# Optimization experiments

Measured on AMD Instinct MI355X. Metric: run time of the kernel, lower is better.

Reference implementation:

```python
import jax, jax.numpy as jnp
import numpy as np

N = 4096
IN_F = 128
OUT_F = 64      # per-head out_features
HEADS = 4
ALPHA = 0.2     # LeakyReLU negative slope
NEG_FILL = -9e15


def setup_inputs() -> dict:
    key = jax.random.key(0)
    k_h, k_adj, k_W, k_a = jax.random.split(key, 4)
    h = jax.random.normal(k_h, (N, IN_F), dtype=jnp.float32)
    adj = jax.random.randint(k_adj, (N, N), 0, 2, dtype=jnp.int32)
    W = jax.random.normal(k_W, (IN_F, OUT_F * HEADS), dtype=jnp.float32) * 0.1
    a = jax.random.normal(k_a, (2 * OUT_F, 1), dtype=jnp.float32) * 0.1
    bias = jnp.zeros((OUT_F * HEADS,), dtype=jnp.float32)
    return {"h": h, "adj": adj, "W": W, "a": a, "bias": bias}


def reference(h, adj, W, a, bias):
    n = h.shape[0]
    Wh = (h @ W).reshape(n, HEADS, OUT_F)            # (N, H, F)
    # e_ij = leakyrelu(a_left . Wh_i + a_right . Wh_j)  (decomposed outer sum;
    # same math as concat([Wh_i, Wh_j]) @ a in the original)
    a_left = a[:OUT_F, 0]                            # (F,)
    a_right = a[OUT_F:, 0]                           # (F,)
    left = jnp.einsum('nhf,f->nh', Wh, a_left)       # (N, H)
    right = jnp.einsum('nhf,f->nh', Wh, a_right)     # (N, H)
    mask = adj > 0                                   # (N, N)
    outs = []
    for head in range(HEADS):                        # small fixed loop over heads
        e = left[:, head, None] + right[None, :, head]          # (N, N)
        e = jnp.where(e >= 0, e, ALPHA * e)                      # LeakyReLU
        e = jnp.where(mask, e, NEG_FILL)
        attn = jax.nn.softmax(e, axis=1)                         # (N, N)
        outs.append(attn @ Wh[:, head, :])                       # (N, F)
    out = jnp.concatenate(outs, axis=1)              # concat=True -> (N, H*F)
    return out + bias
```

## Files before the change

kernel.cpp:

```cpp
#include <hip/hip_runtime.h>
#include <hip/hip_bf16.h>

#define NN 4096
#define IN_F 128
#define OUT_F 64
#define C_TOT 256
#define ALPHA 0.2f
#define LOG2E 1.4426950408889634f

typedef float f32x4 __attribute__((ext_vector_type(4)));
typedef float f32x2 __attribute__((ext_vector_type(2)));
typedef __bf16 bf16x8 __attribute__((ext_vector_type(8)));

__device__ __forceinline__ unsigned fmap(float f) {
    unsigned u = __float_as_uint(f);
    return (u >> 31) ? ~u : (u | 0x80000000u);
}
__device__ __forceinline__ float funmap(unsigned u) {
    return (u >> 31) ? __uint_as_float(u & 0x7FFFFFFFu) : __uint_as_float(~u);
}
__device__ __forceinline__ unsigned short bfbits(float x) {
    union { __bf16 b; unsigned short u; } t;
    t.b = (__bf16)x;
    return t.u;
}
__device__ __forceinline__ void gl16(const void* g, void* l) {
    __builtin_amdgcn_global_load_lds((const __attribute__((address_space(1))) void*)g,
                                     (__attribute__((address_space(3))) void*)l, 16, 0, 0);
}

__global__ __launch_bounds__(256) void k_mask(
    const int* __restrict__ adj, unsigned* __restrict__ mask,
    const float* __restrict__ W, const float* __restrict__ a,
    unsigned short* __restrict__ WTbf, float* __restrict__ uLR,
    unsigned int* __restrict__ Rmax)
{
    const int tid = threadIdx.x;
    const int lane = tid & 63, wv = tid >> 6;
    const int row = blockIdx.x * 4 + wv;
    const int* __restrict__ ar = adj + (size_t)row * NN;
    unsigned* __restrict__ mr = mask + (size_t)row * 128;
    for (int c = 0; c < 8; ++c) {
        const int j0 = c * 512;
        unsigned w = 0u;
#pragma unroll
        for (int k = 0; k < 8; ++k) {
            const unsigned long long bb = __ballot(ar[j0 + k * 64 + lane] > 0);
            const unsigned lo = (unsigned)bb, hi = (unsigned)(bb >> 32);
            if ((lane >> 1) == k) w = (lane & 1) ? hi : lo;
        }
        if (lane < 16) {
            const int wi = c * 16 + lane;
            mr[(wi & 3) * 32 + (wi >> 2)] = w;
        }
    }

    if (blockIdx.x < 32) {
        const int b = blockIdx.x;
        const int c = b * 8 + (tid & 7);
#pragma unroll
        for (int pass = 0; pass < 4; ++pass) {
            const int k = pass * 32 + (tid >> 3);
            WTbf[(size_t)c * IN_F + k] = bfbits(W[k * C_TOT + c]);
        }
        if (b == 0) {
            if (tid < 4) Rmax[tid] = 0u;
            for (int o = tid; o < 1024; o += 256) {
                const int k = o >> 3, j = o & 7;
                const int hd = j & 3, side = j >> 2;
                float s = 0.f;
                for (int f = 0; f < OUT_F; ++f)
                    s = fmaf(W[k * C_TOT + hd * OUT_F + f], a[side * OUT_F + f], s);
                uLR[k * 8 + side * 4 + hd] = s;
            }
        }
    }
}

__global__ __launch_bounds__(256) void k_prep(
    const float* __restrict__ hmat, const unsigned short* __restrict__ WTbf,
    const float* __restrict__ uLR, unsigned short* __restrict__ WhT,
    float* __restrict__ leftT, float* __restrict__ rightT,
    unsigned int* __restrict__ Rmax)
{
    __shared__ float hs[16][132];
    __shared__ float us[128][8];
    const int tid = threadIdx.x;
    const int rowbase = blockIdx.x * 16;

    ((float4*)us)[tid] = ((const float4*)uLR)[tid];
#pragma unroll
    for (int p = 0; p < 8; ++p) {
        const int idx = p * 256 + tid;
        hs[idx >> 7][idx & 127] = hmat[(size_t)rowbase * IN_F + idx];
    }
    __syncthreads();

    const int lane = tid & 63, wv = tid >> 6;
    const int m16 = lane & 15, kg = lane >> 4;

    if (wv == 0) {
        const int row = lane >> 2, hd = lane & 3;
        float aL = 0.f, aR = 0.f;
#pragma unroll
        for (int k = 0; k < 128; k += 4) {
            const float4 hv = *(const float4*)&hs[row][k];
            aL = fmaf(hv.x, us[k][hd],   fmaf(hv.y, us[k+1][hd],   fmaf(hv.z, us[k+2][hd],   fmaf(hv.w, us[k+3][hd],   aL))));
            aR = fmaf(hv.x, us[k][hd+4], fmaf(hv.y, us[k+1][hd+4], fmaf(hv.z, us[k+2][hd+4], fmaf(hv.w, us[k+3][hd+4], aR))));
        }
        leftT [hd * NN + rowbase + row] = aL;
        rightT[hd * NN + rowbase + row] = aR * LOG2E;
        float mx = aR;
#pragma unroll
        for (int s = 4; s < 64; s <<= 1) mx = fmaxf(mx, __shfl_xor(mx, s, 64));
        if (lane < 4) atomicMax(&Rmax[hd], fmap(mx));
    }

    bf16x8 afr[4];
#pragma unroll
    for (int ks = 0; ks < 4; ++ks) {
        const float4 lo = *(const float4*)&hs[m16][ks * 32 + kg * 8];
        const float4 hi = *(const float4*)&hs[m16][ks * 32 + kg * 8 + 4];
        bf16x8 v;
        v[0] = (__bf16)lo.x; v[1] = (__bf16)lo.y; v[2] = (__bf16)lo.z; v[3] = (__bf16)lo.w;
        v[4] = (__bf16)hi.x; v[5] = (__bf16)hi.y; v[6] = (__bf16)hi.z; v[7] = (__bf16)hi.w;
        afr[ks] = v;
    }

#pragma unroll
    for (int nt0 = 0; nt0 < 4; ++nt0) {
        const int col = (wv * 4 + nt0) * 16 + m16;
        f32x4 acc = (f32x4){0.f, 0.f, 0.f, 0.f};
#pragma unroll
        for (int ks = 0; ks < 4; ++ks) {
            union { uint4 u; bf16x8 v; } B;
            B.u = *(const uint4*)(WTbf + (size_t)col * IN_F + ks * 32 + kg * 8);
            acc = __builtin_amdgcn_mfma_f32_16x16x32_bf16(afr[ks], B.v, acc, 0, 0, 0);
        }
#pragma unroll
        for (int i = 0; i < 4; ++i)
            WhT[(size_t)col * NN + rowbase + kg * 4 + i] = bfbits(acc[i]);
    }
}

__global__ __launch_bounds__(512, 6) void k_attn(
    const unsigned* __restrict__ mask,
    const unsigned short* __restrict__ WhT,
    const float* __restrict__ leftT,
    const float* __restrict__ rightT,
    const unsigned int* __restrict__ Rmax,
    const float* __restrict__ bias,
    float* __restrict__ out)
{
    __shared__ unsigned short Bb[2][64 * 128];
    __shared__ float rlds[4096];

    const int tid = threadIdx.x;
    const int lane = tid & 63;
    const int wv = tid >> 6;
    const int rh = wv & 1;
    const int j4 = wv >> 1;
    const int rowbase = (blockIdx.x >> 2) * 32;
    const int hd = blockIdx.x & 3;
    const int m = lane & 15;
    const int kg = lane >> 4;
    const int sh = kg * 8;

#pragma unroll
    for (int p = 0; p < 2; ++p) {
        const int i = p * 512 + tid;
        *(float4*)&rlds[i * 4] = *(const float4*)(rightT + (size_t)hd * NN + i * 4);
    }
    unsigned mreg[32];
    {
        const unsigned* mrow = mask + (size_t)(rowbase + rh * 16 + m) * 128 + j4 * 32;
#pragma unroll
        for (int p = 0; p < 8; ++p) {
            const uint4 v = *(const uint4*)(mrow + p * 4);
            mreg[p * 4 + 0] = v.x; mreg[p * 4 + 1] = v.y;
            mreg[p * 4 + 2] = v.z; mreg[p * 4 + 3] = v.w;
        }
    }

    const float lf = leftT[hd * NN + rowbase + rh * 16 + m];
    const float rmx = funmap(Rmax[hd]);
    const float x = lf + rmx;
    const float m0v = fmaxf(x, ALPHA * x);
    const float mp0 = m0v * LOG2E;
    const float lf2 = fmaf(lf, LOG2E, -mp0);
    const float qc = -0.8f * mp0;
    const f32x2 lf22 = (f32x2){lf2, lf2};
    const f32x2 al2  = (f32x2){ALPHA, ALPHA};
    const f32x2 qc2  = (f32x2){qc, qc};

    bf16x8 ONE8;
#pragma unroll
    for (int i = 0; i < 8; ++i) ONE8[i] = (__bf16)1.0f;

    const int srow0 = wv * 4 + (lane >> 4);
    const int g_lin = lane & 15;
    const int lg = g_lin ^ (srow0 & 15);
    const unsigned short* gsrc0 = WhT + (size_t)(hd * 64 + srow0) * NN + lg * 8;
    const unsigned short* gsrc1 = gsrc0 + (size_t)32 * NN;
    const int d0 = wv * 512 + lane * 8;

#define STAGE(buf, t) {                                  \
    gl16(gsrc0 + (t) * 128, &Bb[buf][d0]);               \
    gl16(gsrc1 + (t) * 128, &Bb[buf][4096 + d0]); }

    const int pg8 = ((j4 * 4 + kg) ^ m) * 8;
    const int bro = m * 128 + pg8;

    f32x4 acc0 = (f32x4){0,0,0,0}, acc1 = acc0, acc2 = acc0, acc3 = acc0;
    f32x4 accL = (f32x4){0,0,0,0};

    union F4 { f32x4 v; f32x2 h[2]; };

#define COMPUTE(buf, t) {                                                        \
    const unsigned aw = mreg[(t)] >> sh;                                         \
    F4 RA, RB;                                                                   \
    RA.v = *(const f32x4*)&rlds[(t) * 128 + j4 * 32 + sh];                       \
    RB.v = *(const f32x4*)&rlds[(t) * 128 + j4 * 32 + sh + 4];                   \
    const f32x2 rp2[4] = { RA.h[0], RA.h[1], RB.h[0], RB.h[1] };                 \
    union { __bf16 b[8]; bf16x8 v; } Af;                                         \
    _Pragma("unroll")                                                            \
    for (int e = 0; e < 4; ++e) {                                                \
        const f32x2 p = rp2[e] + lf22;                         \
        const f32x2 q = __builtin_elementwise_fma(p, al2, qc2);    \
        const float t0 = fmaxf(p.x, q.x), t1 = fmaxf(p.y, q.y);                  \
        float w0 = exp2f(t0), w1 = exp2f(t1);                                    \
        const unsigned mk0 = (unsigned)(((int)(aw << (31 - 2*e)))     >> 31);    \
        const unsigned mk1 = (unsigned)(((int)(aw << (31 - (2*e+1)))) >> 31);    \
        w0 = __uint_as_float(__float_as_uint(w0) & mk0);                         \
        w1 = __uint_as_float(__float_as_uint(w1) & mk1);                         \
        Af.b[2*e]   = (__bf16)w0;                                                \
        Af.b[2*e+1] = (__bf16)w1;                                                \
    }                                                                            \
    union { uint4 u; bf16x8 v; } B0, B1, B2, B3;                                 \
    B0.u = *(const uint4*)&Bb[buf][bro];                                         \
    B1.u = *(const uint4*)&Bb[buf][bro + 2048];                                  \
    B2.u = *(const uint4*)&Bb[buf][bro + 4096];                                  \
    B3.u = *(const uint4*)&Bb[buf][bro + 6144];                                  \
    acc0 = __builtin_amdgcn_mfma_f32_16x16x32_bf16(Af.v, B0.v, acc0, 0, 0, 0);   \
    acc1 = __builtin_amdgcn_mfma_f32_16x16x32_bf16(Af.v, B1.v, acc1, 0, 0, 0);   \
    acc2 = __builtin_amdgcn_mfma_f32_16x16x32_bf16(Af.v, B2.v, acc2, 0, 0, 0);   \
    acc3 = __builtin_amdgcn_mfma_f32_16x16x32_bf16(Af.v, B3.v, acc3, 0, 0, 0);   \
    accL = __builtin_amdgcn_mfma_f32_16x16x32_bf16(Af.v, ONE8, accL, 0, 0, 0);   \
}

    STAGE(0, 0);
    __syncthreads();

#pragma unroll
    for (int t = 0; t < 32; ++t) {
        if (t + 1 < 32) {
            STAGE((t + 1) & 1, t + 1);
            asm volatile("s_waitcnt vmcnt(2)" ::: "memory");
        } else {
            asm volatile("s_waitcnt vmcnt(0)" ::: "memory");
        }
        __builtin_amdgcn_sched_barrier(0);
        COMPUTE(t & 1, t);
        __builtin_amdgcn_sched_barrier(0);
        __builtin_amdgcn_s_barrier();
    }
#undef STAGE
#undef COMPUTE

    __syncthreads();
    float* comb = (float*)&Bb[0][0];
    if (j4 > 0) {
        float* c = comb + (((j4 - 1) * 2 + rh) * 64 + lane) * 20;
#pragma unroll
        for (int i = 0; i < 4; ++i) {
            c[ 0 + i] = acc0[i]; c[ 4 + i] = acc1[i];
            c[ 8 + i] = acc2[i]; c[12 + i] = acc3[i];
            c[16 + i] = accL[i];
        }
    }
    __syncthreads();
    if (j4 == 0) {
#pragma unroll
        for (int pt = 0; pt < 3; ++pt) {
            const float* c = comb + ((pt * 2 + rh) * 64 + lane) * 20;
#pragma unroll
            for (int i = 0; i < 4; ++i) {
                acc0[i] += c[ 0 + i]; acc1[i] += c[ 4 + i];
                acc2[i] += c[ 8 + i]; acc3[i] += c[12 + i];
                accL[i] += c[16 + i];
            }
        }
#pragma unroll
        for (int q = 0; q < 4; ++q) {
            const f32x4 A = (q == 0) ? acc0 : (q == 1) ? acc1 : (q == 2) ? acc2 : acc3;
            const int col = hd * 64 + q * 16 + m;
            const float bv = bias[col];
#pragma unroll
            for (int i = 0; i < 4; ++i) {
                const int r = kg * 4 + i;
                out[(size_t)(rowbase + rh * 16 + r) * C_TOT + col] = A[i] / accL[i] + bv;
            }
        }
    }
}

extern "C" void kernel_launch(void* const* d_in, const int* in_sizes, int n_in,
                              void* d_out, int out_size, void* d_ws, size_t ws_size,
                              hipStream_t stream) {
    const float* hmat = (const float*)d_in[0];
    const int*   adj  = (const int*)d_in[1];
    const float* W    = (const float*)d_in[2];
    const float* a    = (const float*)d_in[3];
    const float* bias = (const float*)d_in[4];
    float* out = (float*)d_out;

    char* ws = (char*)d_ws;
    unsigned short* WhT  = (unsigned short*)(ws + 0x000000);
    float* rightT        = (float*)(ws + 0x280000);
    float* leftT         = (float*)(ws + 0x2A0000);
    unsigned short* WTbf = (unsigned short*)(ws + 0x2B0000);
    float* uLR           = (float*)(ws + 0x2C0000);
    unsigned int* Rmax   = (unsigned int*)(ws + 0x2C1000);
    unsigned* mask       = (unsigned*)(ws + 0x300000);

    hipLaunchKernelGGL(k_mask, dim3(1024), dim3(256), 0, stream,
                       adj, mask, W, a, WTbf, uLR, Rmax);
    hipLaunchKernelGGL(k_prep, dim3(256),  dim3(256), 0, stream,
                       hmat, WTbf, uLR, WhT, leftT, rightT, Rmax);
    hipLaunchKernelGGL(k_attn, dim3(512),  dim3(512), 0, stream,
                       mask, WhT, leftT, rightT, Rmax, bias, out);
}
```

Measured before the change: 71.41 us.

## Split attention key range across two blocks with separate finalize kernel

Splits the column (j) dimension of the attention kernel into two halves, doubling the grid to 1024 blocks. Each block writes unnormalized numerators and row denominators to workspace, and a new finalize kernel sums the halves, divides and adds bias. The aim is more parallelism and occupancy on the 256-CU device, helped by halved LDS for the right vector and a raised launch-bounds occupancy hint. The cost is an extra kernel launch plus extra global traffic for the partial results.

```diff
diff --git a/kernel.cpp b/kernel.cpp
--- a/kernel.cpp
+++ b/kernel.cpp
@@ -143,39 +143,39 @@
     }
 }
 
-__global__ __launch_bounds__(512, 6) void k_attn(
+__global__ __launch_bounds__(512, 8) void k_attn(
     const unsigned* __restrict__ mask,
     const unsigned short* __restrict__ WhT,
     const float* __restrict__ leftT,
     const float* __restrict__ rightT,
     const unsigned int* __restrict__ Rmax,
-    const float* __restrict__ bias,
-    float* __restrict__ out)
+    float* __restrict__ out,
+    float* __restrict__ num1,
+    float* __restrict__ den)
 {
     __shared__ unsigned short Bb[2][64 * 128];
-    __shared__ float rlds[4096];
+    __shared__ float rlds[2048];
 
     const int tid = threadIdx.x;
     const int lane = tid & 63;
     const int wv = tid >> 6;
     const int rh = wv & 1;
     const int j4 = wv >> 1;
-    const int rowbase = (blockIdx.x >> 2) * 32;
-    const int hd = blockIdx.x & 3;
+    const int jh = blockIdx.x & 1;
+    const int hd = (blockIdx.x >> 1) & 3;
+    const int rowbase = (blockIdx.x >> 3) * 32;
     const int m = lane & 15;
     const int kg = lane >> 4;
     const int sh = kg * 8;
 
-#pragma unroll
-    for (int p = 0; p < 2; ++p) {
-        const int i = p * 512 + tid;
-        *(float4*)&rlds[i * 4] = *(const float4*)(rightT + (size_t)hd * NN + i * 4);
-    }
-    unsigned mreg[32];
+    *(float4*)&rlds[tid * 4] =
+        *(const float4*)(rightT + (size_t)hd * NN + jh * 2048 + tid * 4);
+    unsigned mreg[16];
     {
-        const unsigned* mrow = mask + (size_t)(rowbase + rh * 16 + m) * 128 + j4 * 32;
-#pragma unroll
-        for (int p = 0; p < 8; ++p) {
+        const unsigned* mrow = mask + (size_t)(rowbase + rh * 16 + m) * 128
+                               + j4 * 32 + jh * 16;
+#pragma unroll
+        for (int p = 0; p < 4; ++p) {
             const uint4 v = *(const uint4*)(mrow + p * 4);
             mreg[p * 4 + 0] = v.x; mreg[p * 4 + 1] = v.y;
             mreg[p * 4 + 2] = v.z; mreg[p * 4 + 3] = v.w;
@@ -200,7 +200,8 @@
     const int srow0 = wv * 4 + (lane >> 4);
     const int g_lin = lane & 15;
     const int lg = g_lin ^ (srow0 & 15);
-    const unsigned short* gsrc0 = WhT + (size_t)(hd * 64 + srow0) * NN + lg * 8;
+    const unsigned short* gsrc0 = WhT + (size_t)(hd * 64 + srow0) * NN
+                                  + jh * 2048 + lg * 8;
     const unsigned short* gsrc1 = gsrc0 + (size_t)32 * NN;
     const int d0 = wv * 512 + lane * 8;
 
@@ -225,8 +226,8 @@
     union { __bf16 b[8]; bf16x8 v; } Af;                                         \
     _Pragma("unroll")                                                            \
     for (int e = 0; e < 4; ++e) {                                                \
-        const f32x2 p = rp2[e] + lf22;                         \
-        const f32x2 q = __builtin_elementwise_fma(p, al2, qc2);    \
+        const f32x2 p = rp2[e] + lf22;                                           \
+        const f32x2 q = __builtin_elementwise_fma(p, al2, qc2);                  \
         const float t0 = fmaxf(p.x, q.x), t1 = fmaxf(p.y, q.y);                  \
         float w0 = exp2f(t0), w1 = exp2f(t1);                                    \
         const unsigned mk0 = (unsigned)(((int)(aw << (31 - 2*e)))     >> 31);    \
@@ -252,8 +253,8 @@
     __syncthreads();
 
 #pragma unroll
-    for (int t = 0; t < 32; ++t) {
-        if (t + 1 < 32) {
+    for (int t = 0; t < 16; ++t) {
+        if (t + 1 < 16) {
             STAGE((t + 1) & 1, t + 1);
             asm volatile("s_waitcnt vmcnt(2)" ::: "memory");
         } else {
@@ -290,18 +291,43 @@
                 accL[i] += c[16 + i];
             }
         }
+        float* numdst = jh ? num1 : out;
 #pragma unroll
         for (int q = 0; q < 4; ++q) {
             const f32x4 A = (q == 0) ? acc0 : (q == 1) ? acc1 : (q == 2) ? acc2 : acc3;
             const int col = hd * 64 + q * 16 + m;
-            const float bv = bias[col];
 #pragma unroll
             for (int i = 0; i < 4; ++i) {
                 const int r = kg * 4 + i;
-                out[(size_t)(rowbase + rh * 16 + r) * C_TOT + col] = A[i] / accL[i] + bv;
+                numdst[(size_t)(rowbase + rh * 16 + r) * C_TOT + col] = A[i];
             }
         }
-    }
+        if (m == 0) {
+#pragma unroll
+            for (int i = 0; i < 4; ++i)
+                den[(size_t)jh * 4 * NN + hd * NN + rowbase + rh * 16 + kg * 4 + i] = accL[i];
+        }
+    }
+}
+
+__global__ __launch_bounds__(256) void k_fin(
+    float* __restrict__ out, const float* __restrict__ num1,
+    const float* __restrict__ den, const float* __restrict__ bias)
+{
+    const int idx = blockIdx.x * 256 + threadIdx.x;
+    const int row = idx >> 6;
+    const int c4 = (idx & 63) * 4;
+    const int hd = c4 >> 6;
+    const float d = den[hd * NN + row] + den[4 * NN + hd * NN + row];
+    const float rd = 1.0f / d;
+    float4 n0 = *(float4*)(out + (size_t)row * C_TOT + c4);
+    const float4 n1 = *(const float4*)(num1 + (size_t)row * C_TOT + c4);
+    const float4 bv = *(const float4*)(bias + c4);
+    n0.x = fmaf(n0.x + n1.x, rd, bv.x);
+    n0.y = fmaf(n0.y + n1.y, rd, bv.y);
+    n0.z = fmaf(n0.z + n1.z, rd, bv.z);
+    n0.w = fmaf(n0.w + n1.w, rd, bv.w);
+    *(float4*)(out + (size_t)row * C_TOT + c4) = n0;
 }
 
 extern "C" void kernel_launch(void* const* d_in, const int* in_sizes, int n_in,
@@ -322,11 +348,15 @@
     float* uLR           = (float*)(ws + 0x2C0000);
     unsigned int* Rmax   = (unsigned int*)(ws + 0x2C1000);
     unsigned* mask       = (unsigned*)(ws + 0x300000);
+    float* num1          = (float*)(ws + 0x500000);
+    float* den           = (float*)(ws + 0x900000);
 
     hipLaunchKernelGGL(k_mask, dim3(1024), dim3(256), 0, stream,
                        adj, mask, W, a, WTbf, uLR, Rmax);
     hipLaunchKernelGGL(k_prep, dim3(256),  dim3(256), 0, stream,
                        hmat, WTbf, uLR, WhT, leftT, rightT, Rmax);
-    hipLaunchKernelGGL(k_attn, dim3(512),  dim3(512), 0, stream,
-                       mask, WhT, leftT, rightT, Rmax, bias, out);
-}
+    hipLaunchKernelGGL(k_attn, dim3(1024), dim3(512), 0, stream,
+                       mask, WhT, leftT, rightT, Rmax, out, num1, den);
+    hipLaunchKernelGGL(k_fin,  dim3(1024), dim3(256), 0, stream,
+                       out, num1, den, bias);
+}
```

After: 71.34 us. No clear change (-0.1%).

## Factor exp into precomputed per-node terms, split-K attention with final reduction kernel

Applied to the files above, without the earlier changes.

Replaces the per-element exp2 of the LeakyReLU score with products of precomputed exponentials: exp(l+r) and exp(alpha(l+r)) are split into per-row and per-column factors, and their max is taken since exp is monotonic. The attention kernel is restructured so each block handles 64 rows across four 16-row groups over a quarter of the columns. Mask words and exp factors are streamed through LDS with async loads, using a new mask layout. Partial numerators and denominators go to workspace and a new k_fin kernel sums them and normalizes. This removes the transcendental bottleneck and raises MFMA reuse of B tiles, at the cost of extra global traffic for partial sums, an extra launch, and a risk of overflow or underflow in the factored exponentials.

```diff
diff --git a/kernel.cpp b/kernel.cpp
--- a/kernel.cpp
+++ b/kernel.cpp
@@ -9,7 +9,6 @@
 #define LOG2E 1.4426950408889634f
 
 typedef float f32x4 __attribute__((ext_vector_type(4)));
-typedef float f32x2 __attribute__((ext_vector_type(2)));
 typedef __bf16 bf16x8 __attribute__((ext_vector_type(8)));
 
 __device__ __forceinline__ unsigned fmap(float f) {
@@ -28,9 +27,13 @@
     __builtin_amdgcn_global_load_lds((const __attribute__((address_space(1))) void*)g,
                                      (__attribute__((address_space(3))) void*)l, 16, 0, 0);
 }
+__device__ __forceinline__ void gl4(const void* g, void* l) {
+    __builtin_amdgcn_global_load_lds((const __attribute__((address_space(1))) void*)g,
+                                     (__attribute__((address_space(3))) void*)l, 4, 0, 0);
+}
 
 __global__ __launch_bounds__(256) void k_mask(
-    const int* __restrict__ adj, unsigned* __restrict__ mask,
+    const int* __restrict__ adj, unsigned* __restrict__ mask2,
     const float* __restrict__ W, const float* __restrict__ a,
     unsigned short* __restrict__ WTbf, float* __restrict__ uLR,
     unsigned int* __restrict__ Rmax)
@@ -39,7 +42,7 @@
     const int lane = tid & 63, wv = tid >> 6;
     const int row = blockIdx.x * 4 + wv;
     const int* __restrict__ ar = adj + (size_t)row * NN;
-    unsigned* __restrict__ mr = mask + (size_t)row * 128;
+    const int rg = row >> 6, r64 = row & 63;
     for (int c = 0; c < 8; ++c) {
         const int j0 = c * 512;
         unsigned w = 0u;
@@ -51,7 +54,8 @@
         }
         if (lane < 16) {
             const int wi = c * 16 + lane;
-            mr[(wi & 3) * 32 + (wi >> 2)] = w;
+            const int jq = wi >> 5, t = (wi >> 2) & 7, j4 = wi & 3;
+            mask2[(size_t)(((rg * 4 + jq) * 8) + t) * 256 + r64 * 4 + j4] = w;
         }
     }
 
@@ -80,7 +84,7 @@
 __global__ __launch_bounds__(256) void k_prep(
     const float* __restrict__ hmat, const unsigned short* __restrict__ WTbf,
     const float* __restrict__ uLR, unsigned short* __restrict__ WhT,
-    float* __restrict__ leftT, float* __restrict__ rightT,
+    float* __restrict__ leftT, float2* __restrict__ erPair,
     unsigned int* __restrict__ Rmax)
 {
     __shared__ float hs[16][132];
@@ -108,8 +112,9 @@
             aL = fmaf(hv.x, us[k][hd],   fmaf(hv.y, us[k+1][hd],   fmaf(hv.z, us[k+2][hd],   fmaf(hv.w, us[k+3][hd],   aL))));
             aR = fmaf(hv.x, us[k][hd+4], fmaf(hv.y, us[k+1][hd+4], fmaf(hv.z, us[k+2][hd+4], fmaf(hv.w, us[k+3][hd+4], aR))));
         }
-        leftT [hd * NN + rowbase + row] = aL;
-        rightT[hd * NN + rowbase + row] = aR * LOG2E;
+        leftT[hd * NN + rowbase + row] = aL;
+        const float rp = aR * LOG2E;
+        erPair[(size_t)hd * NN + rowbase + row] = make_float2(exp2f(rp), exp2f(ALPHA * rp));
         float mx = aR;
 #pragma unroll
         for (int s = 4; s < 64; s <<= 1) mx = fmaxf(mx, __shfl_xor(mx, s, 64));
@@ -143,119 +148,119 @@
     }
 }
 
-__global__ __launch_bounds__(512, 6) void k_attn(
-    const unsigned* __restrict__ mask,
+__global__ __launch_bounds__(256, 3) void k_attn(
+    const unsigned* __restrict__ mask2,
     const unsigned short* __restrict__ WhT,
     const float* __restrict__ leftT,
-    const float* __restrict__ rightT,
+    const float2* __restrict__ erPair,
     const unsigned int* __restrict__ Rmax,
-    const float* __restrict__ bias,
-    float* __restrict__ out)
+    float* __restrict__ out,
+    float* __restrict__ num123,
+    float* __restrict__ den)
 {
     __shared__ unsigned short Bb[2][64 * 128];
-    __shared__ float rlds[4096];
+    __shared__ float erb[2][256];
+    __shared__ unsigned mb[2][256];
 
     const int tid = threadIdx.x;
     const int lane = tid & 63;
-    const int wv = tid >> 6;
-    const int rh = wv & 1;
-    const int j4 = wv >> 1;
-    const int rowbase = (blockIdx.x >> 2) * 32;
-    const int hd = blockIdx.x & 3;
+    const int j4 = tid >> 6;
+    const int jq = blockIdx.x & 3;
+    const int hd = (blockIdx.x >> 2) & 3;
+    const int rg = blockIdx.x >> 4;
+    const int rowbase = rg * 64;
     const int m = lane & 15;
     const int kg = lane >> 4;
     const int sh = kg * 8;
 
-#pragma unroll
-    for (int p = 0; p < 2; ++p) {
-        const int i = p * 512 + tid;
-        *(float4*)&rlds[i * 4] = *(const float4*)(rightT + (size_t)hd * NN + i * 4);
-    }
-    unsigned mreg[32];
-    {
-        const unsigned* mrow = mask + (size_t)(rowbase + rh * 16 + m) * 128 + j4 * 32;
-#pragma unroll
-        for (int p = 0; p < 8; ++p) {
-            const uint4 v = *(const uint4*)(mrow + p * 4);
-            mreg[p * 4 + 0] = v.x; mreg[p * 4 + 1] = v.y;
-            mreg[p * 4 + 2] = v.z; mreg[p * 4 + 3] = v.w;
-        }
-    }
-
-    const float lf = leftT[hd * NN + rowbase + rh * 16 + m];
+    const int srow4 = j4 * 4 + (lane >> 4);
+    const int g_lin = lane & 15;
+    const int lg = g_lin ^ srow4;
+    const unsigned short* gB = WhT + (size_t)(hd * 64 + srow4) * NN + jq * 1024 + lg * 8;
+    const int dB = srow4 * 128 + g_lin * 8;
+    const char* gE = (const char*)(erPair + (size_t)hd * NN + jq * 1024);
+    const char* gM = (const char*)mask2 + (size_t)((rg * 4 + jq) * 8) * 1024;
+    char* eDst = (char*)&erb[0][0];
+    char* mDst = (char*)&mb[0][0];
+
+#define STAGE(buf, t) {                                                        \
+    gl16(gB + (t) * 128,                      &Bb[buf][dB]);                   \
+    gl16(gB + (t) * 128 + (size_t)16 * NN,    &Bb[buf][dB + 2048]);            \
+    gl16(gB + (t) * 128 + (size_t)32 * NN,    &Bb[buf][dB + 4096]);            \
+    gl16(gB + (t) * 128 + (size_t)48 * NN,    &Bb[buf][dB + 6144]);            \
+    gl4(gE + (t) * 1024 + tid * 4, eDst + (buf) * 1024 + j4 * 256 + lane * 4); \
+    gl4(gM + (t) * 1024 + tid * 4, mDst + (buf) * 1024 + j4 * 256 + lane * 4); }
+
+    STAGE(0, 0);
+
     const float rmx = funmap(Rmax[hd]);
-    const float x = lf + rmx;
-    const float m0v = fmaxf(x, ALPHA * x);
-    const float mp0 = m0v * LOG2E;
-    const float lf2 = fmaf(lf, LOG2E, -mp0);
-    const float qc = -0.8f * mp0;
-    const f32x2 lf22 = (f32x2){lf2, lf2};
-    const f32x2 al2  = (f32x2){ALPHA, ALPHA};
-    const f32x2 qc2  = (f32x2){qc, qc};
-
+    float EL[4], EL2[4];
+#pragma unroll
+    for (int rh = 0; rh < 4; ++rh) {
+        const float lf = leftT[hd * NN + rowbase + rh * 16 + m];
+        const float x = lf + rmx;
+        const float mp0 = fmaxf(x, ALPHA * x) * LOG2E;
+        EL [rh] = exp2f(fmaf(lf,         LOG2E, -mp0));
+        EL2[rh] = exp2f(fmaf(lf * ALPHA, LOG2E, -mp0));
+    }
     bf16x8 ONE8;
 #pragma unroll
     for (int i = 0; i < 8; ++i) ONE8[i] = (__bf16)1.0f;
-
-    const int srow0 = wv * 4 + (lane >> 4);
-    const int g_lin = lane & 15;
-    const int lg = g_lin ^ (srow0 & 15);
-    const unsigned short* gsrc0 = WhT + (size_t)(hd * 64 + srow0) * NN + lg * 8;
-    const unsigned short* gsrc1 = gsrc0 + (size_t)32 * NN;
-    const int d0 = wv * 512 + lane * 8;
-
-#define STAGE(buf, t) {                                  \
-    gl16(gsrc0 + (t) * 128, &Bb[buf][d0]);               \
-    gl16(gsrc1 + (t) * 128, &Bb[buf][4096 + d0]); }
 
     const int pg8 = ((j4 * 4 + kg) ^ m) * 8;
     const int bro = m * 128 + pg8;
 
-    f32x4 acc0 = (f32x4){0,0,0,0}, acc1 = acc0, acc2 = acc0, acc3 = acc0;
-    f32x4 accL = (f32x4){0,0,0,0};
-
-    union F4 { f32x4 v; f32x2 h[2]; };
-
-#define COMPUTE(buf, t) {                                                        \
-    const unsigned aw = mreg[(t)] >> sh;                                         \
-    F4 RA, RB;                                                                   \
-    RA.v = *(const f32x4*)&rlds[(t) * 128 + j4 * 32 + sh];                       \
-    RB.v = *(const f32x4*)&rlds[(t) * 128 + j4 * 32 + sh + 4];                   \
-    const f32x2 rp2[4] = { RA.h[0], RA.h[1], RB.h[0], RB.h[1] };                 \
-    union { __bf16 b[8]; bf16x8 v; } Af;                                         \
-    _Pragma("unroll")                                                            \
-    for (int e = 0; e < 4; ++e) {                                                \
-        const f32x2 p = rp2[e] + lf22;                         \
-        const f32x2 q = __builtin_elementwise_fma(p, al2, qc2);    \
-        const float t0 = fmaxf(p.x, q.x), t1 = fmaxf(p.y, q.y);                  \
-        float w0 = exp2f(t0), w1 = exp2f(t1);                                    \
-        const unsigned mk0 = (unsigned)(((int)(aw << (31 - 2*e)))     >> 31);    \
-        const unsigned mk1 = (unsigned)(((int)(aw << (31 - (2*e+1)))) >> 31);    \
-        w0 = __uint_as_float(__float_as_uint(w0) & mk0);                         \
-        w1 = __uint_as_float(__float_as_uint(w1) & mk1);                         \
-        Af.b[2*e]   = (__bf16)w0;                                                \
-        Af.b[2*e+1] = (__bf16)w1;                                                \
-    }                                                                            \
-    union { uint4 u; bf16x8 v; } B0, B1, B2, B3;                                 \
-    B0.u = *(const uint4*)&Bb[buf][bro];                                         \
-    B1.u = *(const uint4*)&Bb[buf][bro + 2048];                                  \
-    B2.u = *(const uint4*)&Bb[buf][bro + 4096];                                  \
-    B3.u = *(const uint4*)&Bb[buf][bro + 6144];                                  \
-    acc0 = __builtin_amdgcn_mfma_f32_16x16x32_bf16(Af.v, B0.v, acc0, 0, 0, 0);   \
-    acc1 = __builtin_amdgcn_mfma_f32_16x16x32_bf16(Af.v, B1.v, acc1, 0, 0, 0);   \
-    acc2 = __builtin_amdgcn_mfma_f32_16x16x32_bf16(Af.v, B2.v, acc2, 0, 0, 0);   \
-    acc3 = __builtin_amdgcn_mfma_f32_16x16x32_bf16(Af.v, B3.v, acc3, 0, 0, 0);   \
-    accL = __builtin_amdgcn_mfma_f32_16x16x32_bf16(Af.v, ONE8, accL, 0, 0, 0);   \
-}
-
-    STAGE(0, 0);
+    f32x4 acc[4][4], accL[4];
+#pragma unroll
+    for (int rh = 0; rh < 4; ++rh) {
+        accL[rh] = (f32x4){0,0,0,0};
+#pragma unroll
+        for (int q = 0; q < 4; ++q) acc[rh][q] = (f32x4){0,0,0,0};
+    }
+
     __syncthreads();
 
-#pragma unroll
-    for (int t = 0; t < 32; ++t) {
-        if (t + 1 < 32) {
+#define COMPUTE(buf, t) {                                                      \
+    unsigned aw[4];                                                            \
+    _Pragma("unroll")                                                          \
+    for (int rh = 0; rh < 4; ++rh)                                             \
+        aw[rh] = mb[buf][(rh * 16 + m) * 4 + j4] >> sh;                        \
+    const char* eb = (const char*)&erb[buf][0] + j4 * 256 + kg * 64;           \
+    f32x4 V[4];                                                                \
+    _Pragma("unroll")                                                          \
+    for (int c = 0; c < 4; ++c) V[c] = *(const f32x4*)(eb + c * 16);           \
+    union { __bf16 b[8]; bf16x8 v; } Af[4];                                    \
+    _Pragma("unroll")                                                          \
+    for (int rh = 0; rh < 4; ++rh) {                                           \
+        _Pragma("unroll")                                                      \
+        for (int c = 0; c < 4; ++c) {                                          \
+            float w0 = fmaxf(V[c].x * EL[rh], V[c].y * EL2[rh]);               \
+            float w1 = fmaxf(V[c].z * EL[rh], V[c].w * EL2[rh]);               \
+            const unsigned mk0 = (unsigned)(((int)(aw[rh] << (31 - 2*c)))     >> 31); \
+            const unsigned mk1 = (unsigned)(((int)(aw[rh] << (31 - (2*c+1)))) >> 31); \
+            w0 = __uint_as_float(__float_as_uint(w0) & mk0);                   \
+            w1 = __uint_as_float(__float_as_uint(w1) & mk1);                   \
+            Af[rh].b[2*c]   = (__bf16)w0;                                      \
+            Af[rh].b[2*c+1] = (__bf16)w1;                                      \
+        }                                                                      \
+    }                                                                          \
+    union { uint4 u; bf16x8 v; } B[4];                                         \
+    _Pragma("unroll")                                                          \
+    for (int q = 0; q < 4; ++q) B[q].u = *(const uint4*)&Bb[buf][bro + q*2048];\
+    _Pragma("unroll")                                                          \
+    for (int rh = 0; rh < 4; ++rh) {                                           \
+        _Pragma("unroll")                                                      \
+        for (int q = 0; q < 4; ++q)                                            \
+            acc[rh][q] = __builtin_amdgcn_mfma_f32_16x16x32_bf16(Af[rh].v, B[q].v, acc[rh][q], 0, 0, 0); \
+        accL[rh] = __builtin_amdgcn_mfma_f32_16x16x32_bf16(Af[rh].v, ONE8, accL[rh], 0, 0, 0); \
+    }                                                                          \
+}
+
+#pragma unroll
+    for (int t = 0; t < 8; ++t) {
+        if (t < 7) {
             STAGE((t + 1) & 1, t + 1);
-            asm volatile("s_waitcnt vmcnt(2)" ::: "memory");
+            asm volatile("s_waitcnt vmcnt(6)" ::: "memory");
         } else {
             asm volatile("s_waitcnt vmcnt(0)" ::: "memory");
         }
@@ -269,39 +274,74 @@
 
     __syncthreads();
     float* comb = (float*)&Bb[0][0];
-    if (j4 > 0) {
-        float* c = comb + (((j4 - 1) * 2 + rh) * 64 + lane) * 20;
-#pragma unroll
-        for (int i = 0; i < 4; ++i) {
-            c[ 0 + i] = acc0[i]; c[ 4 + i] = acc1[i];
-            c[ 8 + i] = acc2[i]; c[12 + i] = acc3[i];
-            c[16 + i] = accL[i];
-        }
-    }
-    __syncthreads();
+#pragma unroll
+    for (int p = 1; p < 4; ++p) {
+        if (j4 == p) {
+#pragma unroll
+            for (int rh = 0; rh < 4; ++rh) {
+#pragma unroll
+                for (int q = 0; q < 4; ++q)
+                    *(f32x4*)&comb[((rh * 4 + q) * 64 + lane) * 4] = acc[rh][q];
+                *(f32x4*)&comb[((16 + rh) * 64 + lane) * 4] = accL[rh];
+            }
+        }
+        __syncthreads();
+        if (j4 == 0) {
+#pragma unroll
+            for (int rh = 0; rh < 4; ++rh) {
+#pragma unroll
+                for (int q = 0; q < 4; ++q)
+                    acc[rh][q] += *(const f32x4*)&comb[((rh * 4 + q) * 64 + lane) * 4];
+                accL[rh] += *(const f32x4*)&comb[((16 + rh) * 64 + lane) * 4];
+            }
+        }
+        __syncthreads();
+    }
+
     if (j4 == 0) {
-#pragma unroll
-        for (int pt = 0; pt < 3; ++pt) {
-            const float* c = comb + ((pt * 2 + rh) * 64 + lane) * 20;
-#pragma unroll
-            for (int i = 0; i < 4; ++i) {
-                acc0[i] += c[ 0 + i]; acc1[i] += c[ 4 + i];
-                acc2[i] += c[ 8 + i]; acc3[i] += c[12 + i];
-                accL[i] += c[16 + i];
+        float* numdst = (jq == 0) ? out : (num123 + (size_t)(jq - 1) * NN * C_TOT);
+#pragma unroll
+        for (int rh = 0; rh < 4; ++rh) {
+#pragma unroll
+            for (int q = 0; q < 4; ++q) {
+                const int col = hd * 64 + q * 16 + m;
+#pragma unroll
+                for (int i = 0; i < 4; ++i)
+                    numdst[(size_t)(rowbase + rh * 16 + kg * 4 + i) * C_TOT + col] = acc[rh][q][i];
             }
         }
-#pragma unroll
-        for (int q = 0; q < 4; ++q) {
-            const f32x4 A = (q == 0) ? acc0 : (q == 1) ? acc1 : (q == 2) ? acc2 : acc3;
-            const int col = hd * 64 + q * 16 + m;
-            const float bv = bias[col];
-#pragma unroll
-            for (int i = 0; i < 4; ++i) {
-                const int r = kg * 4 + i;
-                out[(size_t)(rowbase + rh * 16 + r) * C_TOT + col] = A[i] / accL[i] + bv;
-            }
-        }
-    }
+        if (m == 0) {
+#pragma unroll
+            for (int rh = 0; rh < 4; ++rh)
+#pragma unroll
+                for (int i = 0; i < 4; ++i)
+                    den[(size_t)(jq * 4 + hd) * NN + rowbase + rh * 16 + kg * 4 + i] = accL[rh][i];
+        }
+    }
+}
+
+__global__ __launch_bounds__(256) void k_fin(
+    float* __restrict__ out, const float* __restrict__ num123,
+    const float* __restrict__ den, const float* __restrict__ bias)
+{
+    const int idx = blockIdx.x * 256 + threadIdx.x;
+    const int row = idx >> 6;
+    const int c4 = (idx & 63) * 4;
+    const int hd = c4 >> 6;
+    const float d = den[(0 * 4 + hd) * NN + row] + den[(1 * 4 + hd) * NN + row]
+                  + den[(2 * 4 + hd) * NN + row] + den[(3 * 4 + hd) * NN + row];
+    const float rd = 1.0f / d;
+    const size_t off = (size_t)row * C_TOT + c4;
+    float4 n = *(float4*)(out + off);
+    const float4 n1 = *(const float4*)(num123 + off);
+    const float4 n2 = *(const float4*)(num123 + (size_t)NN * C_TOT + off);
+    const float4 n3 = *(const float4*)(num123 + (size_t)2 * NN * C_TOT + off);
+    const float4 bv = *(const float4*)(bias + c4);
+    n.x = fmaf(n.x + n1.x + n2.x + n3.x, rd, bv.x);
+    n.y = fmaf(n.y + n1.y + n2.y + n3.y, rd, bv.y);
+    n.z = fmaf(n.z + n1.z + n2.z + n3.z, rd, bv.z);
+    n.w = fmaf(n.w + n1.w + n2.w + n3.w, rd, bv.w);
+    *(float4*)(out + off) = n;
 }
 
 extern "C" void kernel_launch(void* const* d_in, const int* in_sizes, int n_in,
@@ -316,17 +356,21 @@
 
     char* ws = (char*)d_ws;
     unsigned short* WhT  = (unsigned short*)(ws + 0x000000);
-    float* rightT        = (float*)(ws + 0x280000);
     float* leftT         = (float*)(ws + 0x2A0000);
     unsigned short* WTbf = (unsigned short*)(ws + 0x2B0000);
     float* uLR           = (float*)(ws + 0x2C0000);
     unsigned int* Rmax   = (unsigned int*)(ws + 0x2C1000);
-    unsigned* mask       = (unsigned*)(ws + 0x300000);
+    float2* erPair       = (float2*)(ws + 0x2C2000);
+    unsigned* mask2      = (unsigned*)(ws + 0x300000);
+    float* num123        = (float*)(ws + 0x500000);
+    float* den           = (float*)(ws + 0x1100000);
 
     hipLaunchKernelGGL(k_mask, dim3(1024), dim3(256), 0, stream,
-                       adj, mask, W, a, WTbf, uLR, Rmax);
+                       adj, mask2, W, a, WTbf, uLR, Rmax);
     hipLaunchKernelGGL(k_prep, dim3(256),  dim3(256), 0, stream,
-                       hmat, WTbf, uLR, WhT, leftT, rightT, Rmax);
-    hipLaunchKernelGGL(k_attn, dim3(512),  dim3(512), 0, stream,
-                       mask, WhT, leftT, rightT, Rmax, bias, out);
-}
+                       hmat, WTbf, uLR, WhT, leftT, erPair, Rmax);
+    hipLaunchKernelGGL(k_attn, dim3(1024), dim3(256), 0, stream,
+                       mask2, WhT, leftT, erPair, Rmax, out, num123, den);
+    hipLaunchKernelGGL(k_fin,  dim3(1024), dim3(256), 0, stream,
+                       out, num123, den, bias);
+}
```

After: 64.85 us. 9.2% less time.
